# Optimization experiments

Hardware: AMD Instinct MI355X
Metric: run time of the kernel (lower is better)

The kernel has to match this reference:

```python
import jax, jax.numpy as jnp
import numpy as np
import math

B, S, H, NH = 2, 2048, 2048, 16
D = H // NH            # head dim = 128
FF = 4 * H
EPS = 1e-5


def layer_norm(x, w, b):
    mu = jnp.mean(x, axis=-1, keepdims=True)
    var = jnp.mean((x - mu) ** 2, axis=-1, keepdims=True)
    return (x - mu) * jax.lax.rsqrt(var + EPS) * w + b


def rotate_half(x):
    # split last dim into two halves (j=2 grouping), return (-x2, x1)
    x1, x2 = jnp.split(x, 2, axis=-1)
    return jnp.concatenate((-x2, x1), axis=-1)


def rope_freqs(seq_len, dim):
    inv_freq = 1.0 / (10000.0 ** (jnp.arange(0, dim, 2, dtype=jnp.float32) / dim))
    freqs = jnp.arange(seq_len, dtype=jnp.float32)[:, None] * inv_freq[None, :]
    return jnp.concatenate((freqs, freqs), axis=-1)  # [S, D]


def setup_inputs() -> dict:
    key = jax.random.key(0)
    ks = jax.random.split(key, 8)
    sc_h = 1.0 / math.sqrt(H)
    sc_ff = 1.0 / math.sqrt(FF)
    return {
        "hidden_states": jax.random.normal(ks[0], (B, S, H), jnp.float32),
        "attention_mask": jnp.zeros((1, 1, S, S), jnp.bool_),
        "ln1_w": jnp.ones((H,), jnp.float32),
        "ln1_b": jnp.zeros((H,), jnp.float32),
        "wqkv": jax.random.uniform(ks[1], (3 * H, H), jnp.float32, -sc_h, sc_h),
        "bqkv": jnp.zeros((3 * H,), jnp.float32),
        "wdense": jax.random.uniform(ks[2], (H, H), jnp.float32, -sc_h, sc_h),
        "bdense": jnp.zeros((H,), jnp.float32),
        "ln2_w": jnp.ones((H,), jnp.float32),
        "ln2_b": jnp.zeros((H,), jnp.float32),
        "w1": jax.random.uniform(ks[3], (FF, H), jnp.float32, -sc_h, sc_h),
        "b1": jnp.zeros((FF,), jnp.float32),
        "w2": jax.random.uniform(ks[4], (H, FF), jnp.float32, -sc_ff, sc_ff),
        "b2": jnp.zeros((H,), jnp.float32),
    }


def reference(hidden_states, attention_mask, ln1_w, ln1_b, wqkv, bqkv,
              wdense, bdense, ln2_w, ln2_b, w1, b1, w2, b2):
    residual = hidden_states
    x = layer_norm(hidden_states, ln1_w, ln1_b)

    qkv = jnp.einsum('bsh,oh->bso', x, wqkv) + bqkv           # [B,S,3H]
    qkv = qkv.reshape(B, S, NH, 3 * D).transpose(0, 2, 1, 3)  # [B,NH,S,3D]
    q, k, v = jnp.split(qkv, 3, axis=-1)                      # each [B,NH,S,D]

    pos = rope_freqs(S, D)                                    # [S,D]
    cos, sin = jnp.cos(pos), jnp.sin(pos)
    q = q * cos + rotate_half(q) * sin
    k = k * cos + rotate_half(k) * sin

    scale = 1.0 / math.sqrt(D)
    scores = jnp.einsum('bhqd,bhkd->bhqk', q, k) * scale      # [B,NH,S,S]
    causal = jnp.tril(jnp.ones((S, S), jnp.bool_))
    scores = jnp.where(causal, scores.astype(jnp.float32), -1e9)
    probs = jax.nn.softmax(scores, axis=-1).astype(v.dtype)

    ctx = jnp.einsum('bhqk,bhkd->bhqd', probs, v)             # [B,NH,S,D]
    ctx = ctx.transpose(0, 2, 1, 3).reshape(B, S, H)
    attn_out = jnp.einsum('bsh,oh->bso', ctx, wdense) + bdense

    hidden = residual + attn_out
    residual = hidden
    x = layer_norm(hidden, ln2_w, ln2_b)
    inter = jax.nn.gelu(jnp.einsum('bsh,fh->bsf', x, w1) + b1, approximate=False)
    out = jnp.einsum('bsf,hf->bsh', inter, w2) + b2
    hidden = residual + out
    return (hidden, attention_mask)
```

## Files before the change

kernel.cpp:

```cpp
#include <hip/hip_runtime.h>
#include <math.h>

typedef unsigned short u16;
typedef unsigned int u32;
typedef __attribute__((ext_vector_type(8))) __bf16 bf16x8;
typedef __attribute__((ext_vector_type(4))) float f32x4;
typedef __attribute__((ext_vector_type(8))) u16 u16x8;
typedef __attribute__((ext_vector_type(4))) u16 u16x4;

#define BB 2
#define SS 2048
#define HH 2048
#define NHH 16
#define DD 128
#define FFF 8192
#define MM (BB * SS)

__device__ __forceinline__ u16 f2bf(float f) {
  u32 u = __float_as_uint(f);
  u32 r = (u + 0x7FFFu + ((u >> 16) & 1u)) >> 16;
  return (u16)r;
}
__device__ __forceinline__ float b2f(u16 h) {
  return __uint_as_float(((u32)h) << 16);
}
__device__ __forceinline__ void gll16(const void* g, void* l) {
  __builtin_amdgcn_global_load_lds((const __attribute__((address_space(1))) void*)g,
                                   (__attribute__((address_space(3))) void*)l, 16, 0, 0);
}

struct CvtArgs {
  const float* src[4];
  u16* dst[4];
  int n[4];
};
__global__ __launch_bounds__(256) void cvt_all(CvtArgs a) {
  const int seg = blockIdx.y;
  const int i = (blockIdx.x * 256 + threadIdx.x) * 4;
  if (i + 3 < a.n[seg]) {
    f32x4 v = *(const f32x4*)(a.src[seg] + i);
    u16x4 o;
    o[0] = f2bf(v[0]); o[1] = f2bf(v[1]); o[2] = f2bf(v[2]); o[3] = f2bf(v[3]);
    *(u16x4*)(a.dst[seg] + i) = o;
  }
}

__global__ __launch_bounds__(256) void ln_bf16(const float* __restrict__ x,
                                               const float* __restrict__ w,
                                               const float* __restrict__ bsh,
                                               u16* __restrict__ out) {
  const int row = blockIdx.x, tid = threadIdx.x;
  const float* xr = x + (size_t)row * HH;
  f32x4 a = ((const f32x4*)xr)[tid * 2];
  f32x4 b = ((const f32x4*)xr)[tid * 2 + 1];
  float s = a[0] + a[1] + a[2] + a[3] + b[0] + b[1] + b[2] + b[3];
  float q = a[0]*a[0] + a[1]*a[1] + a[2]*a[2] + a[3]*a[3]
          + b[0]*b[0] + b[1]*b[1] + b[2]*b[2] + b[3]*b[3];
#pragma unroll
  for (int off = 32; off > 0; off >>= 1) {
    s += __shfl_down(s, off);
    q += __shfl_down(q, off);
  }
  __shared__ float red[8];
  const int wave = tid >> 6;
  if ((tid & 63) == 0) { red[wave] = s; red[4 + wave] = q; }
  __syncthreads();
  s = red[0] + red[1] + red[2] + red[3];
  q = red[4] + red[5] + red[6] + red[7];
  const float mean = s * (1.0f / HH);
  const float var = q * (1.0f / HH) - mean * mean;
  const float rstd = 1.0f / sqrtf(var + 1e-5f);
  f32x4 w0 = ((const f32x4*)w)[tid * 2];
  f32x4 w1 = ((const f32x4*)w)[tid * 2 + 1];
  f32x4 b0 = ((const f32x4*)bsh)[tid * 2];
  f32x4 b1 = ((const f32x4*)bsh)[tid * 2 + 1];
  u16x8 o;
#pragma unroll
  for (int i = 0; i < 4; ++i) o[i] = f2bf((a[i] - mean) * rstd * w0[i] + b0[i]);
#pragma unroll
  for (int i = 0; i < 4; ++i) o[4 + i] = f2bf((b[i] - mean) * rstd * w1[i] + b1[i]);
  *(u16x8*)(out + (size_t)row * HH + tid * 8) = o;
}

template <int MODE, int DB>
__global__ __launch_bounds__(256) void gemm_bt(const u16* __restrict__ A,
                                               const u16* __restrict__ Bw,
                                               const float* __restrict__ bias,
                                               const float* resid, void* Cout,
                                               int M, int N, int K) {
  __shared__ __align__(16) u16 As[DB ? 2 : 1][128 * 64];
  __shared__ __align__(16) u16 Bs[DB ? 2 : 1][128 * 64];
  const int tid = threadIdx.x;
  const int wave = tid >> 6, lane = tid & 63;
  const int l15 = lane & 15, quad = lane >> 4;
  const int bm = blockIdx.x, bn = blockIdx.y;
  const int wm = (wave >> 1) << 6, wn = (wave & 1) << 6;

  f32x4 acc[4][4] = {};

  const int srow = (wave << 5) + (lane >> 3);
  const int sg = (lane & 7) ^ (lane >> 3);
  const u16* aptr = A + (size_t)(bm * 128 + srow) * K + sg * 8;
  const u16* bptr = Bw + (size_t)(bn * 128 + srow) * K + sg * 8;

  auto stage = [&](int buf) {
#pragma unroll
    for (int i = 0; i < 4; ++i)
      gll16(aptr + (size_t)i * 8 * K, &As[buf][(wave * 4 + i) * 512]);
#pragma unroll
    for (int i = 0; i < 4; ++i)
      gll16(bptr + (size_t)i * 8 * K, &Bs[buf][(wave * 4 + i) * 512]);
    aptr += 64; bptr += 64;
  };

  auto compute = [&](int buf) {
#pragma unroll
    for (int tt = 0; tt < 2; ++tt) {
      bf16x8 af[4], bfv[4];
#pragma unroll
      for (int i = 0; i < 4; ++i) {
        const int m = wm + i * 16 + l15;
        const int n = wn + i * 16 + l15;
        const int gi = tt * 4 + quad;
        af[i] = *(const bf16x8*)&As[buf][m * 64 + ((gi ^ (m & 7)) << 3)];
        bfv[i] = *(const bf16x8*)&Bs[buf][n * 64 + ((gi ^ (n & 7)) << 3)];
      }
#pragma unroll
      for (int i = 0; i < 4; ++i)
#pragma unroll
        for (int j = 0; j < 4; ++j)
          acc[i][j] = __builtin_amdgcn_mfma_f32_16x16x32_bf16(af[i], bfv[j], acc[i][j], 0, 0, 0);
    }
  };

  const int nk = K >> 6;
  if constexpr (DB) {
    stage(0);
    for (int kt = 0; kt < nk; ++kt) {
      __syncthreads();
      if (kt + 1 < nk) stage((kt + 1) & 1);
      compute(kt & 1);
    }
  } else {
    for (int kt = 0; kt < nk; ++kt) {
      stage(0);
      __syncthreads();
      compute(0);
      __syncthreads();
    }
  }

#pragma unroll
  for (int i = 0; i < 4; ++i) {
    const int row0 = bm * 128 + wm + i * 16 + quad * 4;
#pragma unroll
    for (int j = 0; j < 4; ++j) {
      const int col = bn * 128 + wn + j * 16 + l15;
      const float bv = bias[col];
#pragma unroll
      for (int r = 0; r < 4; ++r) {
        const size_t idx = (size_t)(row0 + r) * N + col;
        float v = acc[i][j][r] + bv;
        if constexpr (MODE == 0) {
          ((u16*)Cout)[idx] = f2bf(v);
        } else if constexpr (MODE == 1) {
          ((float*)Cout)[idx] = v + resid[idx];
        } else {
          v = 0.5f * v * (1.0f + erff(v * 0.70710678118654752f));
          ((u16*)Cout)[idx] = f2bf(v);
        }
      }
    }
  }
}

template <int MODE>
__global__ __launch_bounds__(512, 2) void gemm256(const u16* __restrict__ A,
                                                  const u16* __restrict__ Bw,
                                                  const float* __restrict__ bias,
                                                  void* Cout, int M, int N, int K) {
  __shared__ __align__(16) u16 As[2][256 * 64];
  __shared__ __align__(16) u16 Bs[2][256 * 64];
  const int tid = threadIdx.x;
  const int wave = tid >> 6, lane = tid & 63;
  const int l15 = lane & 15, quad = lane >> 4;
  const int wm = wave >> 2, wn = wave & 3;
  const int bm = blockIdx.x, bn = blockIdx.y;

  f32x4 acc[8][4] = {};

  const size_t loff = (size_t)(lane >> 3) * K + (size_t)(((lane & 7) ^ (lane >> 3)) << 3);
  const u16* Abase = A + (size_t)(bm * 256) * K + loff;
  const u16* Bbase = Bw + (size_t)(bn * 256) * K + loff;

  auto stageA = [&](int buf, int kt, int h) {
#pragma unroll
    for (int i = 0; i < 2; ++i) {
      const int c = wave * 2 + i;
      const int rb = ((c & 8) << 4) | (h * 64 + (c & 7) * 8);
      gll16(Abase + (size_t)rb * K + kt * 64, &As[buf][rb * 64]);
    }
  };
  auto stageB = [&](int buf, int kt, int h) {
#pragma unroll
    for (int i = 0; i < 2; ++i) {
      const int c = wave * 2 + i;
      const int rb = (c >> 2) * 64 + h * 32 + (c & 3) * 8;
      gll16(Bbase + (size_t)rb * K + kt * 64, &Bs[buf][rb * 64]);
    }
  };

  auto ldA = [&](const u16* as_, int qm, bf16x8 (&dst)[4][2]) {
#pragma unroll
    for (int im = 0; im < 4; ++im) {
      const int ar = wm * 128 + qm * 64 + im * 16 + l15;
#pragma unroll
      for (int tt = 0; tt < 2; ++tt)
        dst[im][tt] = *(const bf16x8*)&as_[ar * 64 + ((((tt << 2) + quad) ^ (ar & 7)) << 3)];
    }
  };
  auto ldB = [&](const u16* bs_, int qn, bf16x8 (&dst)[2][2]) {
#pragma unroll
    for (int jn = 0; jn < 2; ++jn) {
      const int br = wn * 64 + qn * 32 + jn * 16 + l15;
#pragma unroll
      for (int tt = 0; tt < 2; ++tt)
        dst[jn][tt] = *(const bf16x8*)&bs_[br * 64 + ((((tt << 2) + quad) ^ (br & 7)) << 3)];
    }
  };
  auto mm = [&](bf16x8 (&a)[4][2], bf16x8 (&b)[2][2], int i0, int j0) {
    __builtin_amdgcn_s_setprio(1);
#pragma unroll
    for (int tt = 0; tt < 2; ++tt)
#pragma unroll
      for (int im = 0; im < 4; ++im)
#pragma unroll
        for (int jn = 0; jn < 2; ++jn)
          acc[i0 + im][j0 + jn] = __builtin_amdgcn_mfma_f32_16x16x32_bf16(
              a[im][tt], b[jn][tt], acc[i0 + im][j0 + jn], 0, 0, 0);
    __builtin_amdgcn_s_setprio(0);
  };

  const int nk = K >> 6;
  stageA(0, 0, 0); stageB(0, 0, 0); stageA(0, 0, 1); stageB(0, 0, 1);
  asm volatile("s_waitcnt vmcnt(4)" ::: "memory");
  __builtin_amdgcn_sched_barrier(0);
  __builtin_amdgcn_s_barrier();

  for (int kt = 0; kt < nk; ++kt) {
    const int cb = kt & 1, ob = cb ^ 1;
    const u16* as_ = As[cb];
    const u16* bs_ = Bs[cb];
    const bool pf = (kt + 1 < nk);
    bf16x8 a0[4][2], a1[4][2], b0[2][2], b1[2][2];

    ldA(as_, 0, a0);
    ldB(bs_, 0, b0);
    if (pf) stageA(ob, kt + 1, 0);
    mm(a0, b0, 0, 0);
    if (pf) asm volatile("s_waitcnt vmcnt(4)" ::: "memory");
    else    asm volatile("s_waitcnt vmcnt(2)" ::: "memory");
    __builtin_amdgcn_sched_barrier(0);
    __builtin_amdgcn_s_barrier();

    ldA(as_, 1, a1);
    if (pf) stageB(ob, kt + 1, 0);
    mm(a1, b0, 4, 0);
    if (pf) asm volatile("s_waitcnt vmcnt(4)" ::: "memory");
    else    asm volatile("s_waitcnt vmcnt(0)" ::: "memory");
    __builtin_amdgcn_sched_barrier(0);
    __builtin_amdgcn_s_barrier();

    ldB(bs_, 1, b1);
    if (pf) stageA(ob, kt + 1, 1);
    mm(a1, b1, 4, 2);
    if (pf) stageB(ob, kt + 1, 1);
    mm(a0, b1, 0, 2);
    if (pf) {
      asm volatile("s_waitcnt vmcnt(4)" ::: "memory");
      __builtin_amdgcn_sched_barrier(0);
    }
    __builtin_amdgcn_s_barrier();
  }

#pragma unroll
  for (int i = 0; i < 8; ++i) {
    const int row0 = bm * 256 + wm * 128 + i * 16 + quad * 4;
#pragma unroll
    for (int j = 0; j < 4; ++j) {
      const int col = bn * 256 + wn * 64 + j * 16 + l15;
      const float bv = bias[col];
#pragma unroll
      for (int r = 0; r < 4; ++r) {
        const size_t idx = (size_t)(row0 + r) * N + col;
        float v = acc[i][j][r] + bv;
        if constexpr (MODE == 0) {
          ((u16*)Cout)[idx] = f2bf(v);
        } else {
          v = 0.5f * v * (1.0f + erff(v * 0.70710678118654752f));
          ((u16*)Cout)[idx] = f2bf(v);
        }
      }
    }
  }
}

__global__ __launch_bounds__(256) void rope_kernel(const u16* __restrict__ qkv,
                                                   u16* __restrict__ Qr,
                                                   u16* __restrict__ Kr) {
  const int tid = threadIdx.x;
  const int d = tid & 63;
  const int s = blockIdx.x * 4 + (tid >> 6);
  const int h = blockIdx.y, b = blockIdx.z;
  const u16* row = qkv + ((size_t)(b * SS + s)) * (3 * HH) + h * (3 * DD);
  const float q1 = b2f(row[d]),        q2 = b2f(row[d + 64]);
  const float k1 = b2f(row[DD + d]),   k2 = b2f(row[DD + d + 64]);
  const float inv = expf((float)d * -0.14391156830963714f);
  const float ang = (float)s * inv;
  const float cs = cosf(ang), sn = sinf(ang);
  const size_t o = ((size_t)(b * NHH + h) * SS + s) * DD;
  Qr[o + d]      = f2bf(q1 * cs - q2 * sn);
  Qr[o + d + 64] = f2bf(q2 * cs + q1 * sn);
  Kr[o + d]      = f2bf(k1 * cs - k2 * sn);
  Kr[o + d + 64] = f2bf(k2 * cs + k1 * sn);
}

__device__ __forceinline__ int vslot(int s, int chunk) {
  return chunk ^ (s & 7) ^ ((s >> 3) & 7);
}
__global__ __launch_bounds__(256) void vtrans(const u16* __restrict__ qkv,
                                              u16* __restrict__ Vt) {
  __shared__ __align__(16) u16 Vs[64 * 128];
  const int tid = threadIdx.x;
  const int s0 = blockIdx.x * 64;
  const int bh = blockIdx.y;
  const int b = bh >> 4, h = bh & 15;
  const u16* src = qkv + (size_t)(b * SS + s0) * (3 * HH) + h * (3 * DD) + 2 * DD;
#pragma unroll
  for (int rr = 0; rr < 4; ++rr) {
    const int task = tid + rr * 256;
    const int sr = task >> 4, c = task & 15;
    u16x8 v = *(const u16x8*)(src + (size_t)sr * (3 * HH) + c * 8);
    const int sl = (vslot(sr, c & 7) | (c & 8));
    *(u16x8*)&Vs[sr * 128 + sl * 8] = v;
  }
  __syncthreads();
#pragma unroll
  for (int rr = 0; rr < 4; ++rr) {
    const int task = tid + rr * 256;
    const int dr = task >> 3, c = task & 7;
    u16x8 o;
#pragma unroll
    for (int e = 0; e < 8; ++e) {
      const int s = c * 8 + e;
      const int sl = (vslot(s, dr >> 3 & 7) | ((dr >> 3) & 8));
      o[e] = Vs[s * 128 + sl * 8 + (dr & 7)];
    }
    *(u16x8*)(Vt + (size_t)(bh * DD + dr) * SS + s0 + c * 8) = o;
  }
}

__device__ __forceinline__ void softmax_pv(f32x4 s4[4], bool diag, int qrl0,
                                           float m_run[4], float l_run[4],
                                           f32x4 oacc[8], const u16* vtb,
                                           u16* psw, int quad, int l15) {
  const float SCL = 0.12751742904630190f;
  float pv[4][4];
  float mx[4] = {-3e38f, -3e38f, -3e38f, -3e38f};
#pragma unroll
  for (int jt = 0; jt < 4; ++jt)
#pragma unroll
    for (int r = 0; r < 4; ++r) {
      float sv = s4[jt][r] * SCL;
      if (diag && (jt * 16 + l15) > (qrl0 + r)) sv = -3e38f;
      pv[jt][r] = sv;
      mx[r] = fmaxf(mx[r], sv);
    }
#pragma unroll
  for (int r = 0; r < 4; ++r) {
    mx[r] = fmaxf(mx[r], __shfl_xor(mx[r], 1));
    mx[r] = fmaxf(mx[r], __shfl_xor(mx[r], 2));
    mx[r] = fmaxf(mx[r], __shfl_xor(mx[r], 4));
    mx[r] = fmaxf(mx[r], __shfl_xor(mx[r], 8));
  }
  float al[4];
#pragma unroll
  for (int r = 0; r < 4; ++r) {
    const float mnew = fmaxf(m_run[r], mx[r]);
    al[r] = exp2f(m_run[r] - mnew);
    m_run[r] = mnew;
  }
  float rs[4] = {0.f, 0.f, 0.f, 0.f};
#pragma unroll
  for (int jt = 0; jt < 4; ++jt)
#pragma unroll
    for (int r = 0; r < 4; ++r) {
      const float pp = exp2f(pv[jt][r] - m_run[r]);
      pv[jt][r] = pp;
      rs[r] += pp;
    }
#pragma unroll
  for (int r = 0; r < 4; ++r) {
    rs[r] += __shfl_xor(rs[r], 1);
    rs[r] += __shfl_xor(rs[r], 2);
    rs[r] += __shfl_xor(rs[r], 4);
    rs[r] += __shfl_xor(rs[r], 8);
    l_run[r] = l_run[r] * al[r] + rs[r];
  }
#pragma unroll
  for (int jn = 0; jn < 8; ++jn)
#pragma unroll
    for (int r = 0; r < 4; ++r) oacc[jn][r] *= al[r];
#pragma unroll
  for (int jt = 0; jt < 4; ++jt)
#pragma unroll
    for (int r = 0; r < 4; ++r) {
      const int qr = quad * 4 + r, key = jt * 16 + l15;
      psw[qr * 64 + (((key >> 3) ^ (qr & 7)) << 3) + (key & 7)] = f2bf(pv[jt][r]);
    }
  __threadfence_block();
#pragma unroll
  for (int t = 0; t < 2; ++t) {
    const int gg = t * 4 + quad;
    bf16x8 pf = *(const bf16x8*)&psw[l15 * 64 + ((gg ^ (l15 & 7)) << 3)];
#pragma unroll
    for (int jn = 0; jn < 8; ++jn) {
      const int nd = jn * 16 + l15;
      bf16x8 vf = *(const bf16x8*)&vtb[nd * 64 + ((gg ^ (nd & 7)) << 3)];
      oacc[jn] = __builtin_amdgcn_mfma_f32_16x16x32_bf16(pf, vf, oacc[jn], 0, 0, 0);
    }
  }
}

__global__ __launch_bounds__(256, 2) void attn_kernel(const u16* __restrict__ Q,
                                                      const u16* __restrict__ Kg,
                                                      const u16* __restrict__ Vtg,
                                                      u16* __restrict__ ctx) {
  __shared__ __align__(16) u16 Ks[2][64 * 128];
  __shared__ __align__(16) u16 Vt[2][128 * 64];
  __shared__ __align__(16) u16 Ps[4][16 * 64];
  const int tid = threadIdx.x;
  const int wave = tid >> 6, lane = tid & 63;
  const int l15 = lane & 15, quad = lane >> 4;
  const int p = blockIdx.x, h = blockIdx.y, b = blockIdx.z;
  const int qlo = p, qhi = 31 - p;
  const size_t bh = (size_t)(b * NHH + h);
  const u16* Qp = Q + bh * ((size_t)SS * DD);
  const u16* Kp = Kg + bh * ((size_t)SS * DD);
  const u16* Vp = Vtg + bh * ((size_t)DD * SS);

  bf16x8 qfl[4], qfh[4];
  {
    const u16* ql = Qp + (size_t)(qlo * 64 + wave * 16 + l15) * DD + quad * 8;
    const u16* qh = Qp + (size_t)(qhi * 64 + wave * 16 + l15) * DD + quad * 8;
#pragma unroll
    for (int t = 0; t < 4; ++t) {
      qfl[t] = *(const bf16x8*)(ql + t * 32);
      qfh[t] = *(const bf16x8*)(qh + t * 32);
    }
  }

  f32x4 oal[8] = {}, oah[8] = {};
  float ml[4] = {-3e38f, -3e38f, -3e38f, -3e38f};
  float mh[4] = {-3e38f, -3e38f, -3e38f, -3e38f};
  float ll[4] = {0.f, 0.f, 0.f, 0.f}, lh[4] = {0.f, 0.f, 0.f, 0.f};

  auto stage = [&](int kt, int bufi) {
    const int k0 = kt * 64;
#pragma unroll
    for (int i = 0; i < 4; ++i) {
      const int g = wave * 4 + i;
      const int r = g * 4 + quad;
      const int c = l15 ^ (r & 15);
      gll16(Kp + (size_t)(k0 + r) * DD + c * 8, &Ks[bufi][g * 512]);
    }
#pragma unroll
    for (int i = 0; i < 4; ++i) {
      const int g = wave * 4 + i;
      const int d = g * 8 + (lane >> 3);
      const int c = (lane & 7) ^ (d & 7);
      gll16(Vp + (size_t)d * SS + k0 + c * 8, &Vt[bufi][g * 512]);
    }
  };

  stage(0, 0);
  const int qrl0 = wave * 16 + quad * 4;
  for (int kt = 0; kt <= qhi; ++kt) {
    __syncthreads();
    const u16* ksb = Ks[kt & 1];
    const u16* vtb = Vt[kt & 1];
    if (kt < qhi) stage(kt + 1, (kt + 1) & 1);
    const bool lo = (kt <= qlo);

    f32x4 sh4[4] = {}, sl4[4] = {};
#pragma unroll
    for (int t = 0; t < 4; ++t)
#pragma unroll
      for (int jt = 0; jt < 4; ++jt) {
        const int key = jt * 16 + l15;
        bf16x8 kf = *(const bf16x8*)&ksb[key * 128 + (((t * 4 + quad) ^ (key & 15)) << 3)];
        sh4[jt] = __builtin_amdgcn_mfma_f32_16x16x32_bf16(qfh[t], kf, sh4[jt], 0, 0, 0);
        if (lo) sl4[jt] = __builtin_amdgcn_mfma_f32_16x16x32_bf16(qfl[t], kf, sl4[jt], 0, 0, 0);
      }

    softmax_pv(sh4, kt == qhi, qrl0, mh, lh, oah, vtb, Ps[wave], quad, l15);
    if (lo) softmax_pv(sl4, kt == qlo, qrl0, ml, ll, oal, vtb, Ps[wave], quad, l15);
  }

  float invh[4], invl[4];
#pragma unroll
  for (int r = 0; r < 4; ++r) { invh[r] = 1.0f / lh[r]; invl[r] = 1.0f / ll[r]; }
#pragma unroll
  for (int jn = 0; jn < 8; ++jn)
#pragma unroll
    for (int r = 0; r < 4; ++r) {
      const int col = h * DD + jn * 16 + l15;
      const int rh = qhi * 64 + qrl0 + r;
      const int rl = qlo * 64 + qrl0 + r;
      ctx[(size_t)(b * SS + rh) * HH + col] = f2bf(oah[jn][r] * invh[r]);
      ctx[(size_t)(b * SS + rl) * HH + col] = f2bf(oal[jn][r] * invl[r]);
    }
}

extern "C" void kernel_launch(void* const* d_in, const int* in_sizes, int n_in,
                              void* d_out, int out_size, void* d_ws, size_t ws_size,
                              hipStream_t stream) {
  (void)in_sizes; (void)n_in; (void)ws_size;
  const float* hidden = (const float*)d_in[0];
  const float* ln1w = (const float*)d_in[2];
  const float* ln1b = (const float*)d_in[3];
  const float* wqkv = (const float*)d_in[4];
  const float* bqkv = (const float*)d_in[5];
  const float* wdense = (const float*)d_in[6];
  const float* bdense = (const float*)d_in[7];
  const float* ln2w = (const float*)d_in[8];
  const float* ln2b = (const float*)d_in[9];
  const float* w1 = (const float*)d_in[10];
  const float* b1 = (const float*)d_in[11];
  const float* w2 = (const float*)d_in[12];
  const float* b2 = (const float*)d_in[13];

  char* ws = (char*)d_ws;
  size_t off = 0;
  auto alloc = [&](size_t elems) {
    u16* p = (u16*)(ws + off);
    off += ((elems * 2 + 255) & ~(size_t)255);
    return p;
  };
  u16* wqkvbf = alloc((size_t)3 * HH * HH);
  u16* wdbf   = alloc((size_t)HH * HH);
  u16* w1bf   = alloc((size_t)FFF * HH);
  u16* w2bf   = alloc((size_t)HH * FFF);
  u16* xbf    = alloc((size_t)MM * HH);
  u16* ctx    = alloc((size_t)MM * HH);
  u16* big    = alloc((size_t)MM * 3 * HH + 3 * (size_t)BB * NHH * SS * DD);
  u16* qkvbuf = big;
  u16* Qr = big + (size_t)MM * 3 * HH;
  u16* Kr = Qr + (size_t)BB * NHH * SS * DD;
  u16* Vtg = Kr + (size_t)BB * NHH * SS * DD;
  u16* inter = big;

  CvtArgs ca;
  ca.src[0] = wqkv;   ca.dst[0] = wqkvbf; ca.n[0] = 3 * HH * HH;
  ca.src[1] = wdense; ca.dst[1] = wdbf;   ca.n[1] = HH * HH;
  ca.src[2] = w1;     ca.dst[2] = w1bf;   ca.n[2] = FFF * HH;
  ca.src[3] = w2;     ca.dst[3] = w2bf;   ca.n[3] = HH * FFF;
  cvt_all<<<dim3((FFF * HH) / 1024, 4), 256, 0, stream>>>(ca);

  ln_bf16<<<MM, 256, 0, stream>>>(hidden, ln1w, ln1b, xbf);
  gemm256<0><<<dim3(MM / 256, (3 * HH) / 256), 512, 0, stream>>>(
      xbf, wqkvbf, bqkv, qkvbuf, MM, 3 * HH, HH);
  rope_kernel<<<dim3(SS / 4, NHH, BB), 256, 0, stream>>>(qkvbuf, Qr, Kr);
  vtrans<<<dim3(SS / 64, BB * NHH), 256, 0, stream>>>(qkvbuf, Vtg);
  attn_kernel<<<dim3(16, NHH, BB), 256, 0, stream>>>(Qr, Kr, Vtg, ctx);
  gemm_bt<1, 1><<<dim3(MM / 128, HH / 128), 256, 0, stream>>>(
      ctx, wdbf, bdense, hidden, d_out, MM, HH, HH);
  ln_bf16<<<MM, 256, 0, stream>>>((const float*)d_out, ln2w, ln2b, xbf);
  gemm256<2><<<dim3(MM / 256, FFF / 256), 512, 0, stream>>>(
      xbf, w1bf, b1, inter, MM, FFF, HH);
  gemm_bt<1, 1><<<dim3(MM / 128, HH / 128), 256, 0, stream>>>(
      inter, w2bf, b2, (const float*)d_out, d_out, MM, HH, FFF);

  const size_t hid_elems = (size_t)MM * HH;
  if ((size_t)out_size > hid_elems)
    hipMemsetAsync((char*)d_out + hid_elems * 4, 0,
                   ((size_t)out_size - hid_elems) * 4, stream);
}
```

Measured before the change: 915.3 us.

## Deepen GEMM main loop prefetch with 2x unrolled double-buffer schedule

Restructures the bf16 GEMM main loop into a two-tile unrolled iteration with fixed buffer pointers. Global-to-LDS staging for the next tile now starts one step earlier, so more loads are in flight. Extra barriers and lgkmcnt waits are added around each MFMA cluster. The deeper prefetch is meant to hide global memory latency better, at the cost of more synchronisation points. Correctness depends on the buffer-reuse ordering and assumes nk is even.

```diff
diff --git a/kernel.cpp b/kernel.cpp
--- a/kernel.cpp
+++ b/kernel.cpp
@@ -241,47 +241,82 @@
     __builtin_amdgcn_s_setprio(0);
   };
 
+#define BAR256() __builtin_amdgcn_s_barrier()
+#define LGKM0_256()                                         \
+  do {                                                      \
+    asm volatile("s_waitcnt lgkmcnt(0)" ::: "memory");      \
+    __builtin_amdgcn_sched_barrier(0);                      \
+  } while (0)
+
+  const u16* const As0 = As[0];
+  const u16* const As1 = As[1];
+  const u16* const Bs0 = Bs[0];
+  const u16* const Bs1 = Bs[1];
+
   const int nk = K >> 6;
+  const int niter = nk >> 1;
+
   stageA(0, 0, 0); stageB(0, 0, 0); stageA(0, 0, 1); stageB(0, 0, 1);
-  asm volatile("s_waitcnt vmcnt(4)" ::: "memory");
+  stageA(1, 1, 0); stageB(1, 1, 0); stageA(1, 1, 1);
+  asm volatile("s_waitcnt vmcnt(6)" ::: "memory");
   __builtin_amdgcn_sched_barrier(0);
-  __builtin_amdgcn_s_barrier();
-
-  for (int kt = 0; kt < nk; ++kt) {
-    const int cb = kt & 1, ob = cb ^ 1;
-    const u16* as_ = As[cb];
-    const u16* bs_ = Bs[cb];
-    const bool pf = (kt + 1 < nk);
+  BAR256();
+
+  for (int it = 0; it < niter; ++it) {
+    const int t0 = it * 2, t1 = t0 + 1;
+    const bool pf = (t0 + 2 < nk);
     bf16x8 a0[4][2], a1[4][2], b0[2][2], b1[2][2];
 
-    ldA(as_, 0, a0);
-    ldB(bs_, 0, b0);
-    if (pf) stageA(ob, kt + 1, 0);
+    ldA(As0, 0, a0); ldB(Bs0, 0, b0);
+    stageB(1, t1, 1);
+    asm volatile("s_waitcnt lgkmcnt(8)" ::: "memory");
+    BAR256(); LGKM0_256();
     mm(a0, b0, 0, 0);
-    if (pf) asm volatile("s_waitcnt vmcnt(4)" ::: "memory");
-    else    asm volatile("s_waitcnt vmcnt(2)" ::: "memory");
-    __builtin_amdgcn_sched_barrier(0);
-    __builtin_amdgcn_s_barrier();
-
-    ldA(as_, 1, a1);
-    if (pf) stageB(ob, kt + 1, 0);
+    BAR256();
+    ldA(As0, 1, a1);
+    if (pf) stageA(0, t0 + 2, 0);
+    BAR256(); LGKM0_256();
     mm(a1, b0, 4, 0);
-    if (pf) asm volatile("s_waitcnt vmcnt(4)" ::: "memory");
+    BAR256();
+    ldB(Bs0, 1, b1);
+    if (pf) stageB(0, t0 + 2, 0);
+    BAR256(); LGKM0_256();
+    mm(a1, b1, 4, 2);
+    BAR256();
+    if (pf) stageA(0, t0 + 2, 1);
+    BAR256();
+    mm(a0, b1, 0, 2);
+    if (pf) asm volatile("s_waitcnt vmcnt(6)" ::: "memory");
     else    asm volatile("s_waitcnt vmcnt(0)" ::: "memory");
     __builtin_amdgcn_sched_barrier(0);
-    __builtin_amdgcn_s_barrier();
-
-    ldB(bs_, 1, b1);
-    if (pf) stageA(ob, kt + 1, 1);
+    BAR256();
+
+    ldA(As1, 0, a0); ldB(Bs1, 0, b0);
+    if (pf) stageB(0, t0 + 2, 1);
+    asm volatile("s_waitcnt lgkmcnt(8)" ::: "memory");
+    BAR256(); LGKM0_256();
+    mm(a0, b0, 0, 0);
+    BAR256();
+    ldA(As1, 1, a1);
+    if (pf) stageA(1, t1 + 2, 0);
+    BAR256(); LGKM0_256();
+    mm(a1, b0, 4, 0);
+    BAR256();
+    ldB(Bs1, 1, b1);
+    if (pf) stageB(1, t1 + 2, 0);
+    BAR256(); LGKM0_256();
     mm(a1, b1, 4, 2);
-    if (pf) stageB(ob, kt + 1, 1);
+    BAR256();
+    if (pf) stageA(1, t1 + 2, 1);
+    BAR256();
     mm(a0, b1, 0, 2);
-    if (pf) {
-      asm volatile("s_waitcnt vmcnt(4)" ::: "memory");
-      __builtin_amdgcn_sched_barrier(0);
-    }
-    __builtin_amdgcn_s_barrier();
-  }
+    if (pf) asm volatile("s_waitcnt vmcnt(6)" ::: "memory");
+    else    asm volatile("s_waitcnt vmcnt(0)" ::: "memory");
+    __builtin_amdgcn_sched_barrier(0);
+    BAR256();
+  }
+#undef BAR256
+#undef LGKM0_256
 
 #pragma unroll
   for (int i = 0; i < 8; ++i) {
```

Measured after the change: 923.3 us. No clear change (+0.9%).
